# Optimization experiments

Measured on AMD Instinct MI355X. Metric: run time of the kernel, lower is better.

## Reference

```python
import jax, jax.numpy as jnp
import numpy as np

B = 128
DIM = 1024


def setup_inputs() -> dict:
    key = jax.random.key(0)
    k1, k2 = jax.random.split(key)
    return {
        "input1": jax.random.normal(k1, (B, DIM), dtype=jnp.float32),
        "input2": jax.random.normal(k2, (B, DIM), dtype=jnp.float32),
    }


def reference(input1, input2):
    # Original torch module computes, via a dim x dim x dim permutation tensor:
    #   cc[b, i] = sum_t input1[b, (i - t) % dim] * input2[b, t]   (circular convolution)
    # then sums over the batch and reshapes to [1, 1, dim].
    dim = input1.shape[1]
    # idx[i, t] = (i - t) mod dim  -> circulant gather of input1
    idx = (jnp.arange(dim)[:, None] - jnp.arange(dim)[None, :]) % dim
    gathered = input1[:, idx]                      # [B, dim, dim]
    cc = jnp.einsum('bit,bt->bi', gathered, input2)  # per-batch circular conv [B, dim]
    sum_rep = jnp.sum(cc, axis=0)                  # [dim]
    return sum_rep[None, None, :]                  # [1, 1, dim]
```

## Files before the change

### kernel.cpp

```cpp
#include <hip/hip_runtime.h>


#define CC_D 1024

__device__ __forceinline__ int padf(int f) { return f + (f >> 3); }

__device__ __forceinline__ float bcast(float v, int lane) {
  return __int_as_float(__builtin_amdgcn_readlane(__float_as_int(v), lane));
}

__global__ __launch_bounds__(512, 8) void cc_partial_kernel(
    const float* __restrict__ X, const float* __restrict__ Y,
    float* __restrict__ ws) {
  const int blk    = blockIdx.x;
  const int b      = blk >> 3;
  const int tslice = blk & 7;
  const int tid    = threadIdx.x;
  const int ig     = tid & 127;
  const int ts     = tid >> 7;
  const int lane   = tid & 63;

  __shared__ __align__(16) float smem[4096];
  float4* sm4 = (float4*)smem;

  const int t0 = tslice * 128 + ts * 32;

  float4 xv = make_float4(0.f, 0.f, 0.f, 0.f);
  if (tid < 256) xv = ((const float4*)(X + b * CC_D))[tid];
  const float ymine = Y[b * CC_D + t0 + (lane & 31)];

  if (tid < 256) {
    sm4[padf(tid)]       = xv;
    sm4[padf(tid + 256)] = xv;
  }
  __syncthreads();

  const int f0 = 254 + 2 * ig - (t0 >> 2);

  float W[16];
#pragma unroll
  for (int m = 0; m < 4; ++m) {
    const float4 w = sm4[padf(f0 + m)];
    W[4 * m + 0] = w.x; W[4 * m + 1] = w.y;
    W[4 * m + 2] = w.z; W[4 * m + 3] = w.w;
  }

  float acc[8];
#pragma unroll
  for (int q = 0; q < 8; ++q) acc[q] = 0.f;

#pragma unroll
  for (int g = 0; g < 4; ++g) {
#pragma unroll
    for (int r = 0; r < 8; ++r) {
      const float ybc = bcast(ymine, 8 * g + r);
#pragma unroll
      for (int q = 0; q < 8; ++q)
        acc[q] += W[8 + q - r] * ybc;
    }

    if (g < 3) {
#pragma unroll
      for (int j = 0; j < 8; ++j) W[8 + j] = W[j];
      const float4 w0 = sm4[padf(f0 - 2 * (g + 1))];
      const float4 w1 = sm4[padf(f0 - 2 * (g + 1) + 1)];
      W[0] = w0.x; W[1] = w0.y; W[2] = w0.z; W[3] = w0.w;
      W[4] = w1.x; W[5] = w1.y; W[6] = w1.z; W[7] = w1.w;
    }
  }

  __syncthreads();
  float4* st = (float4*)(smem + ts * CC_D + 8 * ig);
  st[0] = make_float4(acc[0], acc[1], acc[2], acc[3]);
  st[1] = make_float4(acc[4], acc[5], acc[6], acc[7]);
  __syncthreads();

  if (tid < 256) {
    float4 s = make_float4(0.f, 0.f, 0.f, 0.f);
#pragma unroll
    for (int sidx = 0; sidx < 4; ++sidx) {
      const float4 v = ((const float4*)smem)[sidx * 256 + tid];
      s.x += v.x; s.y += v.y; s.z += v.z; s.w += v.w;
    }
    ((float4*)ws)[(size_t)tid * 1024 + blk] = s;
  }
}

__global__ __launch_bounds__(256) void cc_reduce_kernel(
    const float* __restrict__ ws, float* __restrict__ out) {
  const int j   = blockIdx.x;
  const int tid = threadIdx.x;
  const int l   = tid & 63;
  const int w   = tid >> 6;

  __shared__ float4 red[4];

  const float4* row = (const float4*)ws + (size_t)j * 1024;
  float4 s = make_float4(0.f, 0.f, 0.f, 0.f);
#pragma unroll
  for (int c = 0; c < 4; ++c) {
    const float4 v = row[(size_t)(c * 256 + tid)];
    s.x += v.x; s.y += v.y; s.z += v.z; s.w += v.w;
  }
#pragma unroll
  for (int o = 32; o > 0; o >>= 1) {
    s.x += __shfl_xor(s.x, o, 64);
    s.y += __shfl_xor(s.y, o, 64);
    s.z += __shfl_xor(s.z, o, 64);
    s.w += __shfl_xor(s.w, o, 64);
  }
  if (l == 0) red[w] = s;
  __syncthreads();

  if (tid == 0) {
    float4 r = red[0];
    r.x += red[1].x + red[2].x + red[3].x;
    r.y += red[1].y + red[2].y + red[3].y;
    r.z += red[1].z + red[2].z + red[3].z;
    r.w += red[1].w + red[2].w + red[3].w;
    ((float4*)out)[j] = r;
  }
}

extern "C" void kernel_launch(void* const* d_in, const int* in_sizes, int n_in,
                              void* d_out, int out_size, void* d_ws,
                              size_t ws_size, hipStream_t stream) {
  const float* X = (const float*)d_in[0];
  const float* Y = (const float*)d_in[1];
  float* out = (float*)d_out;
  float* ws  = (float*)d_ws;

  cc_partial_kernel<<<1024, 512, 0, stream>>>(X, Y, ws);
  cc_reduce_kernel<<<256, 256, 0, stream>>>(ws, out);
}
```

Measured before the change: 65.98 us.

## Restructure circular-conv partial kernel to 4 outputs per thread, drop LDS reduction

Each thread now computes 4 outputs over 64 t-values instead of 8 outputs over 32, using 256-thread blocks and 2048 blocks. This removes the intra-block shared-memory reduction across t-sub-slices and its extra syncs, and drops the bank-conflict padding. The cost is twice as many workspace partials (2048 per output quad) for the reduce kernel to read, more global traffic, and lower register reuse per LDS load.

```diff
diff --git a/kernel.cpp b/kernel.cpp
--- a/kernel.cpp
+++ b/kernel.cpp
@@ -3,87 +3,63 @@
 
 #define CC_D 1024
 
-__device__ __forceinline__ int padf(int f) { return f + (f >> 3); }
-
 __device__ __forceinline__ float bcast(float v, int lane) {
   return __int_as_float(__builtin_amdgcn_readlane(__float_as_int(v), lane));
 }
 
-__global__ __launch_bounds__(512, 8) void cc_partial_kernel(
+__global__ __launch_bounds__(256, 8) void cc_partial_kernel(
     const float* __restrict__ X, const float* __restrict__ Y,
     float* __restrict__ ws) {
   const int blk    = blockIdx.x;
-  const int b      = blk >> 3;
-  const int tslice = blk & 7;
+  const int b      = blk >> 4;
+  const int tslice = blk & 15;
   const int tid    = threadIdx.x;
-  const int ig     = tid & 127;
-  const int ts     = tid >> 7;
   const int lane   = tid & 63;
 
-  __shared__ __align__(16) float smem[4096];
-  float4* sm4 = (float4*)smem;
+  __shared__ __align__(16) float4 sm4[512];
 
-  const int t0 = tslice * 128 + ts * 32;
+  const int t0 = tslice * 64;
 
-  float4 xv = make_float4(0.f, 0.f, 0.f, 0.f);
-  if (tid < 256) xv = ((const float4*)(X + b * CC_D))[tid];
-  const float ymine = Y[b * CC_D + t0 + (lane & 31)];
-
-  if (tid < 256) {
-    sm4[padf(tid)]       = xv;
-    sm4[padf(tid + 256)] = xv;
-  }
+  const float4 xv   = ((const float4*)(X + b * CC_D))[tid];
+  const float ymine = Y[b * CC_D + t0 + lane];
+  sm4[tid]       = xv;
+  sm4[tid + 256] = xv;
   __syncthreads();
 
-  const int f0 = 254 + 2 * ig - (t0 >> 2);
+  const int fbase = tid + 254 - 16 * tslice;
 
-  float W[16];
-#pragma unroll
-  for (int m = 0; m < 4; ++m) {
-    const float4 w = sm4[padf(f0 + m)];
-    W[4 * m + 0] = w.x; W[4 * m + 1] = w.y;
-    W[4 * m + 2] = w.z; W[4 * m + 3] = w.w;
+  float W[12];
+  {
+    const float4 w0 = sm4[fbase];
+    const float4 w1 = sm4[fbase + 1];
+    const float4 w2 = sm4[fbase + 2];
+    W[0] = w0.x; W[1]  = w0.y; W[2]  = w0.z; W[3]  = w0.w;
+    W[4] = w1.x; W[5]  = w1.y; W[6]  = w1.z; W[7]  = w1.w;
+    W[8] = w2.x; W[9]  = w2.y; W[10] = w2.z; W[11] = w2.w;
   }
 
-  float acc[8];
-#pragma unroll
-  for (int q = 0; q < 8; ++q) acc[q] = 0.f;
+  float4 acc = make_float4(0.f, 0.f, 0.f, 0.f);
 
 #pragma unroll
-  for (int g = 0; g < 4; ++g) {
+  for (int g = 0; g < 8; ++g) {
 #pragma unroll
     for (int r = 0; r < 8; ++r) {
       const float ybc = bcast(ymine, 8 * g + r);
-#pragma unroll
-      for (int q = 0; q < 8; ++q)
-        acc[q] += W[8 + q - r] * ybc;
+      acc.x += W[8 - r]  * ybc;
+      acc.y += W[9 - r]  * ybc;
+      acc.z += W[10 - r] * ybc;
+      acc.w += W[11 - r] * ybc;
     }
-
-    if (g < 3) {
-#pragma unroll
-      for (int j = 0; j < 8; ++j) W[8 + j] = W[j];
-      const float4 w0 = sm4[padf(f0 - 2 * (g + 1))];
-      const float4 w1 = sm4[padf(f0 - 2 * (g + 1) + 1)];
+    if (g < 7) {
+      W[8] = W[0]; W[9] = W[1]; W[10] = W[2]; W[11] = W[3];
+      const float4 w0 = sm4[fbase - 2 * (g + 1)];
+      const float4 w1 = sm4[fbase - 2 * (g + 1) + 1];
       W[0] = w0.x; W[1] = w0.y; W[2] = w0.z; W[3] = w0.w;
       W[4] = w1.x; W[5] = w1.y; W[6] = w1.z; W[7] = w1.w;
     }
   }
 
-  __syncthreads();
-  float4* st = (float4*)(smem + ts * CC_D + 8 * ig);
-  st[0] = make_float4(acc[0], acc[1], acc[2], acc[3]);
-  st[1] = make_float4(acc[4], acc[5], acc[6], acc[7]);
-  __syncthreads();
-
-  if (tid < 256) {
-    float4 s = make_float4(0.f, 0.f, 0.f, 0.f);
-#pragma unroll
-    for (int sidx = 0; sidx < 4; ++sidx) {
-      const float4 v = ((const float4*)smem)[sidx * 256 + tid];
-      s.x += v.x; s.y += v.y; s.z += v.z; s.w += v.w;
-    }
-    ((float4*)ws)[(size_t)tid * 1024 + blk] = s;
-  }
+  ((float4*)ws)[(size_t)tid * 2048 + blk] = acc;
 }
 
 __global__ __launch_bounds__(256) void cc_reduce_kernel(
@@ -95,10 +71,10 @@
 
   __shared__ float4 red[4];
 
-  const float4* row = (const float4*)ws + (size_t)j * 1024;
+  const float4* row = (const float4*)ws + (size_t)j * 2048;
   float4 s = make_float4(0.f, 0.f, 0.f, 0.f);
 #pragma unroll
-  for (int c = 0; c < 4; ++c) {
+  for (int c = 0; c < 8; ++c) {
     const float4 v = row[(size_t)(c * 256 + tid)];
     s.x += v.x; s.y += v.y; s.z += v.z; s.w += v.w;
   }
@@ -130,6 +106,6 @@
   float* out = (float*)d_out;
   float* ws  = (float*)d_ws;
 
-  cc_partial_kernel<<<1024, 512, 0, stream>>>(X, Y, ws);
+  cc_partial_kernel<<<2048, 256, 0, stream>>>(X, Y, ws);
   cc_reduce_kernel<<<256, 256, 0, stream>>>(ws, out);
 }
```

Measured after the change: 70.05 us. +6.2%, slower.
